# Optimization experiments

Hardware: AMD Instinct MI355X
Metric: run time of the kernel (lower is better)

## Reference

```python
import jax, jax.numpy as jnp
import numpy as np


def conv1x1(x, w, b):
    # x: (B, C_in, D, H, W), w: (C_out, C_in), b: (C_out,)  -- 1x1x1 Conv3d == per-voxel linear
    return jnp.einsum('bcdhw,oc->bodhw', x, w) + b[None, :, None, None, None]


def setup_inputs() -> dict:
    key = jax.random.key(0)
    ks = jax.random.split(key, 6)
    B, C, D, H, W = 2, 64, 8, 64, 64
    K = 4096  # codebook_size after halving
    return {
        'z': jax.random.normal(ks[0], (B, C, D, H, W), dtype=jnp.float32),
        'embedding': jax.random.normal(ks[1], (K, C), dtype=jnp.float32),
        'pre_w': jax.random.normal(ks[2], (C, C), dtype=jnp.float32) * (1.0 / np.sqrt(C)),
        'pre_b': jax.random.normal(ks[3], (C,), dtype=jnp.float32) * 0.01,
        'post_w': jax.random.normal(ks[4], (C, C), dtype=jnp.float32) * (1.0 / np.sqrt(C)),
        'post_b': jax.random.normal(ks[5], (C,), dtype=jnp.float32) * 0.01,
    }


def reference(z, embedding, pre_w, pre_b, post_w, post_b):
    B, C, D, H, W = z.shape
    x = conv1x1(z, pre_w, pre_b)  # pre_quant_conv

    # ---- quantize() ----
    # tokens: (B*D*H*W, C)
    t = jnp.transpose(x, (0, 2, 3, 4, 1)).reshape(-1, C)
    # squared euclidean distances (argmin identical to torch.cdist argmin)
    dist2 = (jnp.sum(t * t, axis=-1, keepdims=True)
             - 2.0 * t @ embedding.T
             + jnp.sum(embedding * embedding, axis=-1)[None, :])  # (N, K)
    idx = jnp.argmin(dist2, axis=-1)  # (N,)
    q = embedding[idx]  # gather: (N, C)

    commitment_loss = jnp.mean((jax.lax.stop_gradient(q) - t) ** 2)
    codebook_loss = jnp.mean((q - jax.lax.stop_gradient(t)) ** 2)

    # straight-through estimator
    q = t + jax.lax.stop_gradient(q - t)
    quant = jnp.transpose(q.reshape(B, D, H, W, C), (0, 4, 1, 2, 3))

    out = conv1x1(quant, post_w, post_b)  # post_quant_conv
    indices = idx.reshape(B, D, H, W)
    return out, codebook_loss, commitment_loss, indices
```

## Files before the change

### kernel.cpp

```cpp
#include <hip/hip_runtime.h>
#include <cstdint>
#include <cstddef>

typedef float  f32x4  __attribute__((ext_vector_type(4)));
typedef float  f32x16 __attribute__((ext_vector_type(16)));
typedef short  s16x8  __attribute__((ext_vector_type(8)));

#define DEV __device__ __forceinline__

static constexpr int    DHW       = 32768;
static constexpr int    NTOK      = 65536;
static constexpr int    CHUNK_B   = 18432;
static constexpr size_t OUT_ELEMS = 4194304;
static constexpr float  BIGC      = 512.0f;
static constexpr float  TAU       = 0.015f;
static constexpr int    FLAG_CAP  = 7424;

static constexpr size_t WS_PREP = 0;
static constexpr size_t WS_RESW = 1179648;
static constexpr size_t WS_RESB = 2228224;
static constexpr size_t WS_PART = 2490368;
static constexpr size_t WS_CNT  = 2494464;
static constexpr size_t WS_FLAG = 2494720;

DEV unsigned f2bf(float f) {
  unsigned u = __float_as_uint(f);
  return (u + 0x7FFFu + ((u >> 16) & 1u)) >> 16;
}
DEV float bf2f(unsigned h) { return __uint_as_float(h << 16); }
DEV unsigned med3u(unsigned a, unsigned b, unsigned c) {
  unsigned r;
  asm("v_med3_u32 %0, %1, %2, %3" : "=v"(r) : "v"(a), "v"(b), "v"(c));
  return r;
}
DEV void gl_lds16(const void* g, void* l) {
  __builtin_amdgcn_global_load_lds(
      (const __attribute__((address_space(1))) unsigned int*)g,
      (__attribute__((address_space(3))) unsigned int*)l, 16, 0, 0);
}

__global__ __launch_bounds__(256) void k_pre(const float* __restrict__ z,
    const float* __restrict__ emb, const float* __restrict__ pw, const float* __restrict__ pb,
    float* __restrict__ dout, char* __restrict__ ws)
{
  const int blk = blockIdx.x, tid = threadIdx.x;
  if (blk == 0 && tid == 0) *(int*)(ws + WS_CNT) = 0;
  if (blk < 512) {
    float* t = dout;
    const int v = (blk & 255) * 256 + tid;
    const int half = blk >> 8;
    const int b = v >> 15, r = v & (DHW - 1);
    const float* zp = z + (size_t)b * 64 * DHW + r;
    float zr[64];
#pragma unroll
    for (int c2 = 0; c2 < 64; ++c2) zr[c2] = zp[(size_t)c2 * DHW];
    const int c0 = half * 32;
    for (int c = c0; c < c0 + 32; c += 4) {
      const float* w0 = pw + c * 64;
      const float* w1 = pw + (c + 1) * 64;
      const float* w2 = pw + (c + 2) * 64;
      const float* w3 = pw + (c + 3) * 64;
      float a0 = pb[c], a1 = pb[c + 1], a2 = pb[c + 2], a3 = pb[c + 3];
#pragma unroll
      for (int c2 = 0; c2 < 64; ++c2) {
        const float zv = zr[c2];
        a0 = fmaf(w0[c2], zv, a0); a1 = fmaf(w1[c2], zv, a1);
        a2 = fmaf(w2[c2], zv, a2); a3 = fmaf(w3[c2], zv, a3);
      }
      t[(size_t)c * NTOK + v]       = a0;
      t[(size_t)(c + 1) * NTOK + v] = a1;
      t[(size_t)(c + 2) * NTOK + v] = a2;
      t[(size_t)(c + 3) * NTOK + v] = a3;
    }
  } else {
    const int tt = (blk - 512) * 256 + tid;
#pragma unroll
    for (int uu = 0; uu < 2; ++uu) {
      const int u = tt * 2 + uu;
      const int k = u >> 3, j = u & 7;
      const float* ep = emb + (size_t)k * 64 + j * 8;
      unsigned hw[4], lw[4];
#pragma unroll
      for (int i = 0; i < 4; ++i) {
        float g0 = -2.0f * ep[2 * i], g1 = -2.0f * ep[2 * i + 1];
        unsigned h0 = f2bf(g0); unsigned l0 = f2bf(g0 - bf2f(h0));
        unsigned h1 = f2bf(g1); unsigned l1 = f2bf(g1 - bf2f(h1));
        hw[i] = h0 | (h1 << 16); lw[i] = l0 | (l1 << 16);
      }
      char* base = ws + WS_PREP + (size_t)(k >> 6) * CHUNK_B;
      const int r = k & 63;
      const int swz = (r & 15) << 4;
      char* rowp = base + r * 256;
      *(uint4*)(rowp + ((j * 16) ^ swz))        = make_uint4(hw[0], hw[1], hw[2], hw[3]);
      *(uint4*)(rowp + ((128 + j * 16) ^ swz))  = make_uint4(lw[0], lw[1], lw[2], lw[3]);
      if (j == 0) {
        const float* er = emb + (size_t)k * 64;
        float s = 0.f;
#pragma unroll
        for (int c = 0; c < 64; ++c) s = fmaf(er[c], er[c], s);
        s += BIGC;
        unsigned eh  = f2bf(s);
        float    rs  = s - bf2f(eh);
        unsigned el  = f2bf(rs);
        unsigned el2 = f2bf(rs - bf2f(el));
        *(uint4*)(base + 16384 + r * 16) = make_uint4(eh | (el << 16), el2, 0u, 0u);
        if (r == 0) *(uint4*)(base + 16384 + 1024) = make_uint4(0u, 0u, 0u, 0u);
      }
    }
  }
}

__global__ __launch_bounds__(512, 4) void k_dist(float* __restrict__ dout,
                                                 char* __restrict__ ws)
{
  constexpr int NCH = 32;
  __shared__ __align__(16) char smem[2 * CHUNK_B];
  const float* t = dout;
  const int tid = threadIdx.x;
  const int w = tid >> 6, lane = tid & 63;
  const int l31 = lane & 31, khalf = lane >> 5;
  const int gidx = blockIdx.x >> 1, h = blockIdx.x & 1;
  const int tb = gidx * 256 + w * 32;
  const int tok = tb + l31;

  s16x8 tav[4], tlv[4];
#pragma unroll
  for (int kt = 0; kt < 4; ++kt) {
    const float* tc = t + (size_t)(kt * 16 + khalf * 8) * NTOK + tok;
    float f[8];
#pragma unroll
    for (int i = 0; i < 8; ++i) f[i] = tc[(size_t)i * NTOK];
    union { unsigned u[4]; s16x8 v; } xh, xl;
#pragma unroll
    for (int i = 0; i < 4; ++i) {
      unsigned h0 = f2bf(f[2 * i]),     l0 = f2bf(f[2 * i]     - bf2f(h0));
      unsigned h1 = f2bf(f[2 * i + 1]), l1 = f2bf(f[2 * i + 1] - bf2f(h1));
      xh.u[i] = h0 | (h1 << 16); xl.u[i] = l0 | (l1 << 16);
    }
    tav[kt] = xh.v; tlv[kt] = xl.v;
  }
  s16x8 ones;
  { union { unsigned u[4]; s16x8 v; } o;
    o.u[0] = khalf ? 0u : 0x3F803F80u;
    o.u[1] = khalf ? 0u : 0x00003F80u;
    o.u[2] = 0u; o.u[3] = 0u; ones = o.v; }

  const char* prep = ws + WS_PREP + (size_t)h * NCH * CHUNK_B;
  const int swz = (l31 & 15) << 4;

  {
    const char* src = prep;
    gl_lds16(src + w * 1024 + lane * 16, smem + w * 1024);
    gl_lds16(src + 8192 + w * 1024 + lane * 16, smem + 8192 + w * 1024);
    if (w < 2) gl_lds16(src + 16384 + w * 1024 + lane * 16, smem + 16384 + w * 1024);
  }
  __syncthreads();

  unsigned u1 = 0x7f800000u, u2 = 0x7f800000u;
  int c1 = 0;

  for (int c = 0; c < NCH; ++c) {
    const char* L = smem + (c & 1) * CHUNK_B;
    if (c + 1 < NCH) {
      const char* src = prep + (size_t)(c + 1) * CHUNK_B;
      char* dst = smem + ((c + 1) & 1) * CHUNK_B;
      gl_lds16(src + w * 1024 + lane * 16, dst + w * 1024);
      gl_lds16(src + 8192 + w * 1024 + lane * 16, dst + 8192 + w * 1024);
      if (w < 2) gl_lds16(src + 16384 + w * 1024 + lane * 16, dst + 16384 + w * 1024);
    }
    f32x16 acc0 = {}, acc1 = {};
    {
      const s16x8 e0 = *(const s16x8*)(L + (khalf ? (16384 + 1024) : (16384 + l31 * 16)));
      const s16x8 e1 = *(const s16x8*)(L + (khalf ? (16384 + 1024) : (16384 + (32 + l31) * 16)));
      acc0 = __builtin_amdgcn_mfma_f32_32x32x16_bf16(e0, ones, acc0, 0, 0, 0);
      acc1 = __builtin_amdgcn_mfma_f32_32x32x16_bf16(e1, ones, acc1, 0, 0, 0);
    }
#pragma unroll
    for (int kt = 0; kt < 4; ++kt) {
      const int i0 = (kt * 32 + khalf * 16) ^ swz;
      const s16x8 gh0 = *(const s16x8*)(L + l31 * 256 + i0);
      const s16x8 gl0 = *(const s16x8*)(L + l31 * 256 + (i0 ^ 128));
      const s16x8 gh1 = *(const s16x8*)(L + (32 + l31) * 256 + i0);
      const s16x8 gl1 = *(const s16x8*)(L + (32 + l31) * 256 + (i0 ^ 128));
      acc0 = __builtin_amdgcn_mfma_f32_32x32x16_bf16(gh0, tav[kt], acc0, 0, 0, 0);
      acc0 = __builtin_amdgcn_mfma_f32_32x32x16_bf16(gh0, tlv[kt], acc0, 0, 0, 0);
      acc0 = __builtin_amdgcn_mfma_f32_32x32x16_bf16(gl0, tav[kt], acc0, 0, 0, 0);
      acc1 = __builtin_amdgcn_mfma_f32_32x32x16_bf16(gh1, tav[kt], acc1, 0, 0, 0);
      acc1 = __builtin_amdgcn_mfma_f32_32x32x16_bf16(gh1, tlv[kt], acc1, 0, 0, 0);
      acc1 = __builtin_amdgcn_mfma_f32_32x32x16_bf16(gl1, tav[kt], acc1, 0, 0, 0);
    }
    const unsigned p1 = u1;
#pragma unroll
    for (int q = 0; q < 16; ++q) {
      const unsigned w0 = (unsigned)((q & 3) + 8 * (q >> 2));
      unsigned v0 = (__float_as_uint(acc0[q]) & ~63u) | w0;
      u2 = med3u(u1, v0, u2); u1 = u1 < v0 ? u1 : v0;
      unsigned v1 = (__float_as_uint(acc1[q]) & ~63u) | (w0 + 32u);
      u2 = med3u(u1, v1, u2); u1 = u1 < v1 ? u1 : v1;
    }
    if (u1 != p1) c1 = c;
    __syncthreads();
  }

  u1 |= (unsigned)(khalf * 4);
  const unsigned o1 = __shfl_xor(u1, 32);
  const unsigned o2 = __shfl_xor(u2, 32);
  const int      oc = __shfl_xor(c1, 32);
  const unsigned am = u1 & ~63u, om = o1 & ~63u;
  const int mycode = c1 * 64 + (int)(u1 & 63u);
  const int ocode  = oc * 64 + (int)(o1 & 63u);
  const bool owins = (om < am) || (om == am && ocode < mycode);
  const unsigned f1 = owins ? o1 : u1;
  const int      fc = owins ? oc : c1;
  const unsigned mx = owins ? am : om;
  unsigned s2 = (u2 & ~63u) < (o2 & ~63u) ? (u2 & ~63u) : (o2 & ~63u);
  s2 = s2 < mx ? s2 : mx;
  if (khalf == 0) {
    const bool nt = (__uint_as_float(s2) - __uint_as_float(f1 & ~63u)) < TAU;
    ((unsigned*)(ws + WS_RESW))[h * 65536 + tok] = f1;
    ((unsigned char*)(ws + WS_RESB))[h * 65536 + tok] =
        (unsigned char)(fc | (nt ? 0x80 : 0));
  }
}

__global__ __launch_bounds__(256) void k_merge(const float* __restrict__ emb,
    float* __restrict__ dout, char* __restrict__ ws)
{
  __shared__ float ls[4];
  const int tid = threadIdx.x;
  const int v = blockIdx.x * 64 + (tid >> 2);
  const int q4 = tid & 3;
  const unsigned* resw = (const unsigned*)(ws + WS_RESW);
  const unsigned char* resb = (const unsigned char*)(ws + WS_RESB);
  const unsigned A = resw[v], B = resw[65536 + v];
  const unsigned am = A & ~63u, bm = B & ~63u;
  const bool bwins = bm < am;
  const unsigned bw = bwins ? B : A;
  const int bq = bwins ? 1 : 0;
  const unsigned k1 = bwins ? bm : am;
  const unsigned k2 = bwins ? am : bm;
  const unsigned char bb = resb[bq * 65536 + v];
  const int code = bq * 2048 + (int)(bb & 31u) * 64 + (int)(bw & 63u);
  const float* tcol = dout + v;
  const float* qe = emb + (size_t)code * 64 + q4 * 16;
  float acc = 0.f;
#pragma unroll
  for (int i = 0; i < 4; ++i) {
    const float4 qv = *(const float4*)(qe + i * 4);
#pragma unroll
    for (int j = 0; j < 4; ++j) {
      const int ch = q4 * 16 + i * 4 + j;
      const float d = tcol[(size_t)ch * NTOK] - ((const float*)&qv)[j];
      acc = fmaf(d, d, acc);
    }
  }
  acc += __shfl_xor(acc, 1);
  acc += __shfl_xor(acc, 2);
  if (q4 == 0) {
    dout[OUT_ELEMS + 2 + v] = (float)code;
    const bool flag = (bb & 0x80u) ||
                      (__uint_as_float(k2) - __uint_as_float(k1) < TAU);
    if (flag) {
      int p = atomicAdd((int*)(ws + WS_CNT), 1);
      if (p < FLAG_CAP) ((int*)(ws + WS_FLAG))[p] = v;
    }
  }
#pragma unroll
  for (int m = 4; m < 64; m <<= 1) acc += __shfl_xor(acc, m);
  const int lane = tid & 63, wv = tid >> 6;
  if (lane == 0) ls[wv] = acc;
  __syncthreads();
  if (tid == 0)
    ((float*)(ws + WS_PART))[blockIdx.x] = ls[0] + ls[1] + ls[2] + ls[3];
}

__global__ __launch_bounds__(256) void k_refine(const float* __restrict__ z,
    const float* __restrict__ emb, const float* __restrict__ pw, const float* __restrict__ pb,
    float* __restrict__ dout, char* __restrict__ ws)
{
  __shared__ double tdsh[64];
  __shared__ double dred[4]; __shared__ int kred[4];
  int cv = *(const int*)(ws + WS_CNT);
  if (cv > FLAG_CAP) cv = FLAG_CAP;
  const int tid = threadIdx.x;
  const int lane = tid & 63, wv = tid >> 6;

  for (int slot = blockIdx.x; slot < cv; slot += 256) {
    const int n = ((const int*)(ws + WS_FLAG))[slot];

    if (tid < 64) {
      const int b = n >> 15, r = n & (DHW - 1);
      const float* zp = z + (size_t)b * 64 * DHW + r;
      const float* wr = pw + tid * 64;
      double a = (double)pb[tid];
      for (int c2 = 0; c2 < 64; ++c2)
        a = fma((double)wr[c2], (double)zp[(size_t)c2 * DHW], a);
      tdsh[tid] = a;
    }
    __syncthreads();

    double td[64];
#pragma unroll
    for (int j = 0; j < 64; ++j) td[j] = tdsh[j];

    double dmin = 1e300; int kmin = 0;
    for (int it = 0; it < 16; ++it) {
      const int code = it * 256 + tid;
      const float4* e = (const float4*)(emb + (size_t)code * 64);
      double d0 = 0.0, d1 = 0.0;
#pragma unroll
      for (int i = 0; i < 16; ++i) {
        const float4 ev = e[i];
        const double x0 = td[4 * i]     - (double)ev.x; d0 = fma(x0, x0, d0);
        const double x1 = td[4 * i + 1] - (double)ev.y; d1 = fma(x1, x1, d1);
        const double x2 = td[4 * i + 2] - (double)ev.z; d0 = fma(x2, x2, d0);
        const double x3 = td[4 * i + 3] - (double)ev.w; d1 = fma(x3, x3, d1);
      }
      const double d = d0 + d1;
      if (d < dmin) { dmin = d; kmin = code; }
    }
#pragma unroll
    for (int m = 1; m < 64; m <<= 1) {
      const double od = __shfl_xor(dmin, m);
      const int    ok = __shfl_xor(kmin, m);
      if (od < dmin || (od == dmin && ok < kmin)) { dmin = od; kmin = ok; }
    }
    if (lane == 0) { dred[wv] = dmin; kred[wv] = kmin; }
    __syncthreads();
    if (tid == 0) {
#pragma unroll
      for (int i = 1; i < 4; ++i)
        if (dred[i] < dmin || (dred[i] == dmin && kred[i] < kmin)) { dmin = dred[i]; kmin = kred[i]; }
      dout[OUT_ELEMS + 2 + n] = (float)kmin;
    }
    __syncthreads();
  }
}

__global__ __launch_bounds__(256) void k_post(const float* __restrict__ emb,
    const float* __restrict__ ow, const float* __restrict__ ob,
    float* __restrict__ dout, const char* __restrict__ ws)
{
  __shared__ float ps[256];
  const int v = (blockIdx.x & 255) * 256 + threadIdx.x;
  const int half = blockIdx.x >> 8;
  const int b = v >> 15, r = v & (DHW - 1);
  const int code = (int)dout[OUT_ELEMS + 2 + v];
  const float* q = emb + (size_t)code * 64;
  float qr[64];
#pragma unroll
  for (int i = 0; i < 16; ++i) *(float4*)(qr + i * 4) = *(const float4*)(q + i * 4);
  float* op = dout + (size_t)b * 64 * DHW + r;
  const int o0 = half * 32;
  for (int o = o0; o < o0 + 32; o += 4) {
    const float* w0 = ow + o * 64;
    const float* w1 = ow + (o + 1) * 64;
    const float* w2 = ow + (o + 2) * 64;
    const float* w3 = ow + (o + 3) * 64;
    float a0 = ob[o], a1 = ob[o + 1], a2 = ob[o + 2], a3 = ob[o + 3];
#pragma unroll
    for (int cch = 0; cch < 64; ++cch) {
      const float qv = qr[cch];
      a0 = fmaf(w0[cch], qv, a0); a1 = fmaf(w1[cch], qv, a1);
      a2 = fmaf(w2[cch], qv, a2); a3 = fmaf(w3[cch], qv, a3);
    }
    op[(size_t)o * DHW]       = a0;
    op[(size_t)(o + 1) * DHW] = a1;
    op[(size_t)(o + 2) * DHW] = a2;
    op[(size_t)(o + 3) * DHW] = a3;
  }
  if (blockIdx.x == 0) {
    const float* part = (const float*)(ws + WS_PART);
    const int t4 = threadIdx.x * 4;
    float s = ((part[t4] + part[t4 + 1]) + part[t4 + 2]) + part[t4 + 3];
    ps[threadIdx.x] = s;
    __syncthreads();
    if (threadIdx.x == 0) {
      float tot = 0.f;
      for (int i = 0; i < 256; ++i) tot += ps[i];
      const float mean = tot / 4194304.0f;
      dout[OUT_ELEMS]     = mean;
      dout[OUT_ELEMS + 1] = mean;
    }
  }
}

extern "C" void kernel_launch(void* const* d_in, const int* in_sizes, int n_in,
                              void* d_out, int out_size, void* d_ws, size_t ws_size,
                              hipStream_t stream) {
  (void)in_sizes; (void)n_in; (void)out_size; (void)ws_size;
  const float* z   = (const float*)d_in[0];
  const float* emb = (const float*)d_in[1];
  const float* pw  = (const float*)d_in[2];
  const float* pb  = (const float*)d_in[3];
  const float* ow  = (const float*)d_in[4];
  const float* ob  = (const float*)d_in[5];
  float* out = (float*)d_out;
  char*  ws  = (char*)d_ws;

  hipLaunchKernelGGL(k_pre,    dim3(576),  dim3(256), 0, stream, z, emb, pw, pb, out, ws);
  hipLaunchKernelGGL(k_dist,   dim3(512),  dim3(512), 0, stream, out, ws);
  hipLaunchKernelGGL(k_merge,  dim3(1024), dim3(256), 0, stream, emb, out, ws);
  hipLaunchKernelGGL(k_refine, dim3(256),  dim3(256), 0, stream, z, emb, pw, pb, out, ws);
  hipLaunchKernelGGL(k_post,   dim3(512),  dim3(256), 0, stream, emb, ow, ob, out, ws);
}
```

Before: 180.8 us.

## Widen distance blocks to 16 waves and split codebook into four quarters

The distance kernel now runs 1024-thread blocks covering 512 tokens each, and the codebook is split across four block groups instead of two, so each block walks 16 chunks instead of 32. Each staged codebook chunk in LDS is shared by twice as many waves, and one load instruction per wave now covers the full row region, which cuts global-to-LDS staging work per token. The merge kernel is extended to take the best and second-best over four partial results and to decode the narrower chunk index. The risk is register pressure and occupancy under the larger block with the stricter launch bound, and the longer four-way merge.

```diff
diff --git a/kernel.cpp b/kernel.cpp
--- a/kernel.cpp
+++ b/kernel.cpp
@@ -110,17 +110,17 @@
   }
 }
 
-__global__ __launch_bounds__(512, 4) void k_dist(float* __restrict__ dout,
-                                                 char* __restrict__ ws)
+__global__ __launch_bounds__(1024, 4) void k_dist(float* __restrict__ dout,
+                                                  char* __restrict__ ws)
 {
-  constexpr int NCH = 32;
+  constexpr int NCH = 16;
   __shared__ __align__(16) char smem[2 * CHUNK_B];
   const float* t = dout;
   const int tid = threadIdx.x;
   const int w = tid >> 6, lane = tid & 63;
   const int l31 = lane & 31, khalf = lane >> 5;
-  const int gidx = blockIdx.x >> 1, h = blockIdx.x & 1;
-  const int tb = gidx * 256 + w * 32;
+  const int gidx = blockIdx.x >> 2, h = blockIdx.x & 3;
+  const int tb = gidx * 512 + w * 32;
   const int tok = tb + l31;
 
   s16x8 tav[4], tlv[4];
@@ -148,12 +148,13 @@
   const char* prep = ws + WS_PREP + (size_t)h * NCH * CHUNK_B;
   const int swz = (l31 & 15) << 4;
 
-  {
-    const char* src = prep;
-    gl_lds16(src + w * 1024 + lane * 16, smem + w * 1024);
-    gl_lds16(src + 8192 + w * 1024 + lane * 16, smem + 8192 + w * 1024);
-    if (w < 2) gl_lds16(src + 16384 + w * 1024 + lane * 16, smem + 16384 + w * 1024);
-  }
+  auto stage = [&](int cc) {
+    const char* src = prep + (size_t)cc * CHUNK_B;
+    char* dst = smem + (size_t)(cc & 1) * CHUNK_B;
+    gl_lds16(src + w * 1024 + lane * 16, dst + w * 1024);
+    if (w < 2) gl_lds16(src + 16384 + w * 1024 + lane * 16, dst + 16384 + w * 1024);
+  };
+  stage(0);
   __syncthreads();
 
   unsigned u1 = 0x7f800000u, u2 = 0x7f800000u;
@@ -161,13 +162,7 @@
 
   for (int c = 0; c < NCH; ++c) {
     const char* L = smem + (c & 1) * CHUNK_B;
-    if (c + 1 < NCH) {
-      const char* src = prep + (size_t)(c + 1) * CHUNK_B;
-      char* dst = smem + ((c + 1) & 1) * CHUNK_B;
-      gl_lds16(src + w * 1024 + lane * 16, dst + w * 1024);
-      gl_lds16(src + 8192 + w * 1024 + lane * 16, dst + 8192 + w * 1024);
-      if (w < 2) gl_lds16(src + 16384 + w * 1024 + lane * 16, dst + 16384 + w * 1024);
-    }
+    if (c + 1 < NCH) stage(c + 1);
     f32x16 acc0 = {}, acc1 = {};
     {
       const s16x8 e0 = *(const s16x8*)(L + (khalf ? (16384 + 1024) : (16384 + l31 * 16)));
@@ -232,15 +227,16 @@
   const int q4 = tid & 3;
   const unsigned* resw = (const unsigned*)(ws + WS_RESW);
   const unsigned char* resb = (const unsigned char*)(ws + WS_RESB);
-  const unsigned A = resw[v], B = resw[65536 + v];
-  const unsigned am = A & ~63u, bm = B & ~63u;
-  const bool bwins = bm < am;
-  const unsigned bw = bwins ? B : A;
-  const int bq = bwins ? 1 : 0;
-  const unsigned k1 = bwins ? bm : am;
-  const unsigned k2 = bwins ? am : bm;
+  unsigned k1 = 0xffffffffu, k2 = 0xffffffffu, bw = 0; int bq = 0;
+#pragma unroll
+  for (int q = 0; q < 4; ++q) {
+    const unsigned W = resw[q * 65536 + v];
+    const unsigned key = W & ~63u;
+    if (key < k1) { k2 = k1; k1 = key; bq = q; bw = W; }
+    else          { k2 = key < k2 ? key : k2; }
+  }
   const unsigned char bb = resb[bq * 65536 + v];
-  const int code = bq * 2048 + (int)(bb & 31u) * 64 + (int)(bw & 63u);
+  const int code = bq * 1024 + (int)(bb & 15u) * 64 + (int)(bw & 63u);
   const float* tcol = dout + v;
   const float* qe = emb + (size_t)code * 64 + q4 * 16;
   float acc = 0.f;
@@ -398,9 +394,9 @@
   float* out = (float*)d_out;
   char*  ws  = (char*)d_ws;
 
-  hipLaunchKernelGGL(k_pre,    dim3(576),  dim3(256), 0, stream, z, emb, pw, pb, out, ws);
-  hipLaunchKernelGGL(k_dist,   dim3(512),  dim3(512), 0, stream, out, ws);
-  hipLaunchKernelGGL(k_merge,  dim3(1024), dim3(256), 0, stream, emb, out, ws);
-  hipLaunchKernelGGL(k_refine, dim3(256),  dim3(256), 0, stream, z, emb, pw, pb, out, ws);
-  hipLaunchKernelGGL(k_post,   dim3(512),  dim3(256), 0, stream, emb, ow, ob, out, ws);
-}
+  hipLaunchKernelGGL(k_pre,    dim3(576),  dim3(256),  0, stream, z, emb, pw, pb, out, ws);
+  hipLaunchKernelGGL(k_dist,   dim3(512),  dim3(1024), 0, stream, out, ws);
+  hipLaunchKernelGGL(k_merge,  dim3(1024), dim3(256),  0, stream, emb, out, ws);
+  hipLaunchKernelGGL(k_refine, dim3(256),  dim3(256),  0, stream, z, emb, pw, pb, out, ws);
+  hipLaunchKernelGGL(k_post,   dim3(512),  dim3(256),  0, stream, emb, ow, ob, out, ws);
+}
```

Result: no change. 179.4 us (-0.8%).
